# Performance work log

Hardware: AMD Instinct MI355X
Metric: run time of the kernel (lower is better)

The kernel has to match this reference:

```python
import jax, jax.numpy as jnp
import numpy as np

N, E = 50000, 200000          # nodes, edges
S, V = 256, 128               # 256x0e scalars, 128x1o vectors -> node dim 640
EDGE_DIM, HID = 64, 256
NUM_ATOM, NUM_BOND = 16, 5
FAN_TP = S * S + V * V        # fully-connected TP fan-in for rescale


def setup_inputs() -> dict:
    key = jax.random.key(0)
    ks = jax.random.split(key, 12)
    h_final = jax.random.normal(ks[0], (N, S + 3 * V), dtype=jnp.float32)
    e_final = jax.random.normal(ks[1], (E, EDGE_DIM), dtype=jnp.float32)
    target_node_mask = jnp.ones((N,), dtype=bool)
    target_edge_mask = jnp.ones((E,), dtype=bool)
    edge_index = jax.random.randint(ks[2], (2, E), 0, N)

    def lin(k, o, i):
        return (jax.random.normal(k, (o, i), jnp.float32) / np.sqrt(i)).astype(jnp.float32)

    return {
        "h_final": h_final,
        "e_final": e_final,
        "target_node_mask": target_node_mask,
        "target_edge_mask": target_edge_mask,
        "edge_index": edge_index,
        "Ws_w": lin(ks[3], S, S),          # LinearRS on scalar irreps (with bias)
        "Ws_b": jnp.zeros((S,), jnp.float32),
        "Wv": lin(ks[4], V, V),            # LinearRS on 1o irreps (no bias)
        "Wcoord": (jax.random.normal(ks[5], (V,), jnp.float32) / np.sqrt(V)),  # 128x1o -> 1x1o
        "W_tp00": jax.random.normal(ks[6], (S, S), jnp.float32),  # 0e x 0e -> 0e path weights
        "W_tp11": jax.random.normal(ks[7], (V, V), jnp.float32),  # 1o x 1o -> 0e path weights
        "atom_W1": lin(ks[8], HID, S), "atom_b1": jnp.zeros((HID,), jnp.float32),
        "atom_W2": lin(ks[9], NUM_ATOM, HID), "atom_b2": jnp.zeros((NUM_ATOM,), jnp.float32),
        "bond_W1": lin(ks[10], HID, 1 + EDGE_DIM), "bond_b1": jnp.zeros((HID,), jnp.float32),
        "bond_W2": lin(ks[11], NUM_BOND, HID), "bond_b2": jnp.zeros((NUM_BOND,), jnp.float32),
    }


def reference(h_final, e_final, target_node_mask, target_edge_mask, edge_index,
              Ws_w, Ws_b, Wv, Wcoord, W_tp00, W_tp11,
              atom_W1, atom_b1, atom_W2, atom_b2,
              bond_W1, bond_b1, bond_W2, bond_b2):
    # --- node heads (masks are all-True here; boolean gather kept for faithfulness) ---
    x = h_final[target_node_mask]                 # [Nt, 640]
    xs = x[:, :S]                                 # scalar (0e) part [Nt, 256]
    xv = x[:, S:].reshape(-1, V, 3)               # vector (1o) part [Nt, 128, 3]

    scalar_feats = xs @ Ws_w.T + Ws_b             # node_scalar_proj (LinearRS)
    atom_type_logits = jax.nn.silu(scalar_feats @ atom_W1.T + atom_b1) @ atom_W2.T + atom_b2

    vec = jnp.einsum('nci,dc->ndi', xv, Wv)       # node_vector_proj, per-component channel mix
    predicted_r0 = jnp.einsum('nci,c->ni', vec, Wcoord)  # coord_head -> [Nt, 3]

    # --- bond head: edge gather + fully-connected tensor product to 0e ---
    ei = edge_index[:, target_edge_mask]
    row, col = ei[0], ei[1]
    hr, hc = h_final[row], h_final[col]           # [Et, 640] each
    sr, sc = hr[:, :S], hc[:, :S]
    vr = hr[:, S:].reshape(-1, V, 3)
    vc = hc[:, S:].reshape(-1, V, 3)
    # paths: 0e(x)0e->0e and 1o(x)1o->0e (dot product, CG norm 1/sqrt(3)), rescaled by fan-in
    tp = (jnp.einsum('ei,ej,ij->e', sr, sc, W_tp00)
          + jnp.einsum('eci,edi,cd->e', vr, vc, W_tp11) / np.sqrt(3.0)) / np.sqrt(FAN_TP)
    bond_in = jnp.concatenate([tp[:, None], e_final[target_edge_mask]], axis=-1)  # [Et, 65]
    bond_logits = jax.nn.silu(bond_in @ bond_W1.T + bond_b1) @ bond_W2.T + bond_b2

    return atom_type_logits, predicted_r0, bond_logits
```

## Files before the change

### kernel.cpp

```cpp
#include <hip/hip_runtime.h>

typedef unsigned short u16;
typedef unsigned int u32;
typedef float f32x4 __attribute__((ext_vector_type(4)));
typedef float f32x2 __attribute__((ext_vector_type(2)));
typedef short s16x8 __attribute__((ext_vector_type(8)));
typedef __bf16 bf16x8 __attribute__((ext_vector_type(8)));

#define NNODE 50000
#define NEDGE 200000
#define INV_SQRT3 0.57735026918962576f
#define INV_SQRT_FAN 0.0034938562148434216f

__device__ inline float b2f(u16 x) {
    unsigned u = ((unsigned)x) << 16;
    return __builtin_bit_cast(float, u);
}
__device__ inline u16 f2b(float f) {
    unsigned u = __builtin_bit_cast(unsigned, f);
    unsigned r = u + 0x7FFFu + ((u >> 16) & 1u);
    return (u16)(r >> 16);
}
__device__ inline float silu(float v) { return v / (1.f + __expf(-v)); }

__device__ inline float ld1(const void* p, long i, int m) {
    return m ? ((const float*)p)[i] : b2f(((const u16*)p)[i]);
}
__device__ inline void stout(void* o, long i, float v, int m) {
    if (m) ((float*)o)[i] = v; else ((u16*)o)[i] = f2b(v);
}

#if defined(__has_builtin)
# if __has_builtin(__builtin_amdgcn_cvt_pk_f32_fp8) && __has_builtin(__builtin_amdgcn_cvt_pk_fp8_f32)
#  define HAVE_FP8 1
# endif
#endif
#ifndef HAVE_FP8
# define HAVE_FP8 0
#endif

__device__ inline int f2e4m3_soft(float f) {
    unsigned u = __builtin_bit_cast(unsigned, f);
    int s = (u >> 24) & 0x80;
    float a = __builtin_fabsf(f);
    if (a >= 464.f) return s | 0x7E;
    if (a < 0.015625f) {
        int q = (int)(a * 512.f + 0.5f);
        return s | q;
    }
    int e = (int)((u >> 23) & 0xFF) - 127;
    unsigned m = u & 0x7FFFFF;
    unsigned mq = (m + 0x80000) >> 20;
    if (mq == 8) { mq = 0; e += 1; }
    if (e > 8) return s | 0x7E;
    return s | ((e + 7) << 3) | (int)mq;
}
__device__ inline float e4m3f_soft(int b) {
    int em = b & 0x7F;
    float v;
    if (em >> 3) {
        unsigned bits = ((unsigned)((em >> 3) + 120) << 23) | ((unsigned)(em & 7) << 20);
        v = __builtin_bit_cast(float, bits);
    } else {
        v = (float)em * 0.001953125f;
    }
    return (b & 0x80) ? -v : v;
}
__device__ inline int enc2(float a, float b) {
#if HAVE_FP8
    return __builtin_amdgcn_cvt_pk_fp8_f32(a, b, 0, false) & 0xFFFF;
#else
    return f2e4m3_soft(a) | (f2e4m3_soft(b) << 8);
#endif
}
__device__ inline unsigned char enc1(float a) { return (unsigned char)(enc2(a, a) & 0xFF); }

__device__ inline float dot8(unsigned p, unsigned x, float acc) {
#if HAVE_FP8
    f32x2 p0 = __builtin_amdgcn_cvt_pk_f32_fp8((int)p, false);
    f32x2 p1 = __builtin_amdgcn_cvt_pk_f32_fp8((int)p, true);
    f32x2 x0 = __builtin_amdgcn_cvt_pk_f32_fp8((int)x, false);
    f32x2 x1 = __builtin_amdgcn_cvt_pk_f32_fp8((int)x, true);
    return acc + p0.x * x0.x + p0.y * x0.y + p1.x * x1.x + p1.y * x1.y;
#else
    float r = acc;
#pragma unroll
    for (int i = 0; i < 4; ++i)
        r += e4m3f_soft((p >> (8 * i)) & 0xFF) * e4m3f_soft((x >> (8 * i)) & 0xFF);
    return r;
#endif
}

template <typename V>
__device__ auto mfma_sel(V a, V b, f32x4 c, int)
    -> decltype(__builtin_amdgcn_mfma_f32_16x16x32_bf16(a, b, c, 0, 0, 0)) {
    return __builtin_amdgcn_mfma_f32_16x16x32_bf16(a, b, c, 0, 0, 0);
}
template <typename V>
__device__ f32x4 mfma_sel(V a, V b, f32x4 c, long) {
    bf16x8 aa = __builtin_bit_cast(bf16x8, a);
    bf16x8 bb = __builtin_bit_cast(bf16x8, b);
    return __builtin_amdgcn_mfma_f32_16x16x32_bf16(aa, bb, c, 0, 0, 0);
}
__device__ inline f32x4 mfma_bf16(s16x8 a, s16x8 b, f32x4 c) {
    return mfma_sel(a, b, c, 0);
}

typedef __attribute__((address_space(1))) u32 AS1u32;
typedef __attribute__((address_space(3))) u32 AS3u32;
__device__ __forceinline__ void async16(const void* g, void* l) {
    __builtin_amdgcn_global_load_lds((AS1u32*)g, (AS3u32*)l, 16, 0, 0);
}

__global__ __launch_bounds__(256) void detect_k(const void* __restrict__ h, int* __restrict__ flag) {
    int t = threadIdx.x;
    u16 w = ((const u16*)h)[2 * t];
    int tb = (w >> 8) & 0x7F;
    bool pl = (tb >= 0x38 && tb <= 0x41);
    unsigned long long b = __ballot(pl);
    __shared__ int cnt[4];
    if ((t & 63) == 0) cnt[t >> 6] = __popcll(b);
    __syncthreads();
    if (t == 0) {
        int s = cnt[0] + cnt[1] + cnt[2] + cnt[3];
        flag[0] = (s < 128) ? 1 : 0;
    }
}

__global__ __launch_bounds__(256) void prep_misc_k(
    const void* __restrict__ W00, const void* __restrict__ W11,
    const void* __restrict__ bW1, const void* __restrict__ Wv,
    const void* __restrict__ Wcoord, const void* __restrict__ aW2,
    const void* __restrict__ bW2, const void* __restrict__ bb1,
    u16* __restrict__ W00T, u16* __restrict__ W1p, u16* __restrict__ W2p,
    float* __restrict__ w1tp, float* __restrict__ w_eff,
    u16* __restrict__ W2ah, u16* __restrict__ W11T, float* __restrict__ b1f,
    const int* __restrict__ mflag)
{
    const int m = *mflag;
    int u = blockIdx.x * 256 + threadIdx.x;
    if (u < 65536) {
        int j = u >> 8, i = u & 255;
        W00T[u] = f2b(ld1(W00, (long)i * 256 + j, m));
    } else if (u < 81920) {
        int v = u - 65536;
        int j = v & 7, ln = (v >> 3) & 63, tk = v >> 9;
        int tn = tk >> 1, kt = tk & 1;
        int hrow = tn * 16 + (ln & 15);
        int k = kt * 32 + (ln >> 4) * 8 + j;
        W1p[v] = f2b(ld1(bW1, (long)hrow * 65 + 1 + k, m));
    } else if (u < 86016) {
        int v = u - 81920;
        int j = v & 7, ln = (v >> 3) & 63, kt = v >> 9;
        int o = ln & 15;
        int k = kt * 32 + (ln >> 4) * 8 + j;
        W2p[v] = (o < 5) ? f2b(ld1(bW2, (long)o * 256 + k, m)) : (u16)0;
    } else if (u < 86272) {
        int hd = u - 86016;
        w1tp[hd] = ld1(bW1, (long)hd * 65, m);
    } else if (u < 86400) {
        int c = u - 86272;
        float acc = 0.f;
        for (int d = 0; d < 128; ++d)
            acc += ld1(Wcoord, d, m) * ld1(Wv, (long)d * 128 + c, m);
        w_eff[c] = acc;
    } else if (u < 90496) {
        int v = u - 86400;
        W2ah[v] = f2b(ld1(aW2, v, m));
    } else if (u < 106880) {
        int v = u - 90496;
        int d = v >> 7, c = v & 127;
        W11T[v] = f2b(ld1(W11, (long)c * 128 + d, m));
    } else if (u < 107136) {
        int hd = u - 106880;
        b1f[hd] = ld1(bb1, hd, m);
    }
}

__global__ __launch_bounds__(256) void prep_w1s_k(
    const void* __restrict__ aW1, const void* __restrict__ Wsw,
    const void* __restrict__ Wsb, const void* __restrict__ ab1,
    u16* __restrict__ W1sh, float* __restrict__ b1p,
    const int* __restrict__ mflag)
{
    const int m = *mflag;
    int hd = blockIdx.x, s = threadIdx.x;
    float acc = 0.f;
    for (int j = 0; j < 256; ++j)
        acc += ld1(aW1, (long)hd * 256 + j, m) * ld1(Wsw, (long)j * 256 + s, m);
    W1sh[hd * 256 + s] = f2b(acc);
    if (s == 0) {
        float b = ld1(ab1, hd, m);
        for (int j = 0; j < 256; ++j)
            b += ld1(aW1, (long)hd * 256 + j, m) * ld1(Wsb, j, m);
        b1p[hd] = b;
    }
}

__global__ __launch_bounds__(256) void zero_k(float4* __restrict__ p) {
    int t = blockIdx.x * 256 + threadIdx.x;
    if (t < 200000) p[t] = float4{0.f, 0.f, 0.f, 0.f};
}

__device__ __forceinline__ void gemm_core_128(
    const u16* __restrict__ Aptr, int lda,
    const u16* __restrict__ Bt, int ldb, int bcol0,
    long bm0, int K, u16* __restrict__ S, f32x4 acc[4][4])
{
    u16* As = S;
    u16* Bs = S + 8192;
    int tid = threadIdx.x;
    int lane = tid & 63, wave = tid >> 6;
    int sr = lane >> 2, sc = (lane & 3) * 8;

    auto stage = [&](int buf, int k0) {
#pragma unroll
        for (int i = 0; i < 2; ++i) {
            int row = wave * 32 + i * 16 + sr;
            async16(Bt + (long)(bcol0 + row) * ldb + k0 + sc,
                    Bs + buf * 4096 + wave * 1024 + i * 512);
            long grow = bm0 + row; if (grow >= NNODE) grow = NNODE - 1;
            async16(Aptr + grow * (long)lda + k0 + sc,
                    As + buf * 4096 + wave * 1024 + i * 512);
        }
    };

    int NT = K >> 5;
    stage(0, 0);
    __syncthreads();
    int wm = (wave & 1) * 64, wn = (wave >> 1) * 64;
    int lm = lane & 15, quad = lane >> 4;
    for (int t = 0; t < NT; ++t) {
        int cur = t & 1;
        if (t + 1 < NT) stage(cur ^ 1, (t + 1) * 32);
        const u16* Ac = As + cur * 4096;
        const u16* Bc = Bs + cur * 4096;
        s16x8 af[4], bfr[4];
#pragma unroll
        for (int q = 0; q < 4; ++q) {
            af[q]  = *(const s16x8*)(Ac + (wm + q * 16 + lm) * 32 + quad * 8);
            bfr[q] = *(const s16x8*)(Bc + (wn + q * 16 + lm) * 32 + quad * 8);
        }
#pragma unroll
        for (int i = 0; i < 4; ++i)
#pragma unroll
            for (int j = 0; j < 4; ++j)
                acc[i][j] = mfma_bf16(af[i], bfr[j], acc[i][j]);
        __syncthreads();
    }
}

__global__ __launch_bounds__(256) void mlp1_k(
    const u16* __restrict__ Xs16, const u16* __restrict__ Bh,
    const float* __restrict__ b1p, const u16* __restrict__ W2ah,
    float* __restrict__ outP)
{
    __shared__ __align__(16) u16 S[17408];
    int bid = blockIdx.x;
    int x = bid & 7, s = bid >> 3;
    int rb = (s >> 1) * 8 + x, cb = s & 1;
    if (rb >= 391) return;
    long bm0 = (long)rb * 128;
    int bn0 = cb * 128;
    f32x4 acc[4][4] = {};
    gemm_core_128(Xs16, 256, Bh, 256, bn0, bm0, 256, S, acc);

    int tid = threadIdx.x, lane = tid & 63, wave = tid >> 6;
    int wm = (wave & 1) * 64, wn = (wave >> 1) * 64;
    int lm = lane & 15, quad = lane >> 4;
#pragma unroll
    for (int j = 0; j < 4; ++j) {
        int col = wn + j * 16 + lm;
        float bb = b1p[bn0 + col];
#pragma unroll
        for (int i = 0; i < 4; ++i)
#pragma unroll
            for (int rr = 0; rr < 4; ++rr)
                S[(wm + i * 16 + quad * 4 + rr) * 136 + col] = f2b(silu(acc[i][j][rr] + bb));
    }
    __syncthreads();
    const u16* wp = W2ah + lm * 256 + bn0;
#pragma unroll
    for (int rg = 0; rg < 2; ++rg) {
        int r0 = wave * 32 + rg * 16;
        f32x4 a2 = {0.f, 0.f, 0.f, 0.f};
#pragma unroll
        for (int k0 = 0; k0 < 128; k0 += 32) {
            s16x8 a = *(const s16x8*)(S + (r0 + lm) * 136 + k0 + quad * 8);
            s16x8 b = *(const s16x8*)(wp + k0 + quad * 8);
            a2 = mfma_bf16(a, b, a2);
        }
#pragma unroll
        for (int rr = 0; rr < 4; ++rr) {
            long grow = bm0 + r0 + quad * 4 + rr;
            if (grow < NNODE)
                atomicAdd(outP + grow * 16 + lm, a2[rr]);
        }
    }
}

__global__ __launch_bounds__(256) void fin_atom_k(
    const float* __restrict__ outP, const void* __restrict__ b2v,
    void* __restrict__ out, const int* __restrict__ mflag)
{
    const int m = *mflag;
    int t4 = blockIdx.x * 256 + threadIdx.x;
    if (t4 >= 200000) return;
    float4 v = *(const float4*)(outP + (long)t4 * 4);
    int b0i = (t4 * 4) & 15;
    float r0 = v.x + ld1(b2v, b0i + 0, m);
    float r1 = v.y + ld1(b2v, b0i + 1, m);
    float r2 = v.z + ld1(b2v, b0i + 2, m);
    float r3 = v.w + ld1(b2v, b0i + 3, m);
    if (m) {
        *(float4*)((float*)out + (long)t4 * 4) = float4{r0, r1, r2, r3};
    } else {
        u16 pk[4] = {f2b(r0), f2b(r1), f2b(r2), f2b(r3)};
        *(ushort4*)((u16*)out + (long)t4 * 4) = *(const ushort4*)pk;
    }
}

__global__ __launch_bounds__(256) void packx8_k(
    const void* __restrict__ h, u16* __restrict__ xvp,
    const float* __restrict__ w_eff, unsigned char* __restrict__ X8,
    u16* __restrict__ Xs16, void* __restrict__ out,
    const int* __restrict__ mflag)
{
    const int m = *mflag;
    int lane = threadIdx.x & 63, w = threadIdx.x >> 6;
    int node = blockIdx.x * 4 + w;
    if (node >= NNODE) return;
    float s4[4];
    if (m) {
        float4 v = *(const float4*)((const float*)h + (long)node * 640 + lane * 4);
        s4[0] = v.x; s4[1] = v.y; s4[2] = v.z; s4[3] = v.w;
    } else {
        ushort4 v = *(const ushort4*)((const u16*)h + (long)node * 640 + lane * 4);
        s4[0] = b2f(v.x); s4[1] = b2f(v.y); s4[2] = b2f(v.z); s4[3] = b2f(v.w);
    }
    unsigned sp = (unsigned)enc2(s4[0], s4[1]) | ((unsigned)enc2(s4[2], s4[3]) << 16);
    *(unsigned*)(X8 + (long)node * 640 + lane * 4) = sp;
    u16 sx[4] = {f2b(s4[0]), f2b(s4[1]), f2b(s4[2]), f2b(s4[3])};
    *(ushort4*)(Xs16 + (long)node * 256 + lane * 4) = *(const ushort4*)sx;
    float a[6];
    if (m) {
        const float* p = (const float*)h + (long)node * 640 + 256 + lane * 6;
        float2 v0 = *(const float2*)p;
        float2 v1 = *(const float2*)(p + 2);
        float2 v2 = *(const float2*)(p + 4);
        a[0] = v0.x; a[1] = v0.y; a[2] = v1.x; a[3] = v1.y; a[4] = v2.x; a[5] = v2.y;
    } else {
        const u16* p = (const u16*)h + (long)node * 640 + 256 + lane * 6;
        ushort2 v0 = *(const ushort2*)p;
        ushort2 v1 = *(const ushort2*)(p + 2);
        ushort2 v2 = *(const ushort2*)(p + 4);
        a[0] = b2f(v0.x); a[1] = b2f(v0.y); a[2] = b2f(v1.x);
        a[3] = b2f(v1.y); a[4] = b2f(v2.x); a[5] = b2f(v2.y);
    }
#pragma unroll
    for (int z = 0; z < 3; ++z) {
        unsigned pk = (unsigned)f2b(a[z]) | ((unsigned)f2b(a[z + 3]) << 16);
        *(unsigned*)(xvp + (long)z * 6400000 + (long)node * 128 + lane * 2) = pk;
        *(unsigned short*)(X8 + (long)node * 640 + 256 + z * 128 + lane * 2) =
            (unsigned short)enc2(a[z], a[z + 3]);
    }
    float2 we = *(const float2*)(w_eff + lane * 2);
    float s0 = a[0] * we.x + a[3] * we.y;
    float s1 = a[1] * we.x + a[4] * we.y;
    float s2 = a[2] * we.x + a[5] * we.y;
#pragma unroll
    for (int off = 32; off > 0; off >>= 1) {
        s0 += __shfl_down(s0, off);
        s1 += __shfl_down(s1, off);
        s2 += __shfl_down(s2, off);
    }
    if (lane == 0) {
        stout(out, 800000L + (long)node * 3 + 0, s0, m);
        stout(out, 800000L + (long)node * 3 + 1, s1, m);
        stout(out, 800000L + (long)node * 3 + 2, s2, m);
    }
}

__global__ __launch_bounds__(256) void gemm8n_k(
    const u16* __restrict__ Xs16, const u16* __restrict__ xvp,
    const u16* __restrict__ W00T, const u16* __restrict__ W11T,
    unsigned char* __restrict__ PQ8, float s00, float s11)
{
    __shared__ __align__(16) u16 S[16384];
    int bid = blockIdx.x;
    int x = bid & 7, s = bid >> 3;
    int rb = (s / 5) * 8 + x, cb = s % 5;
    if (rb >= 391) return;
    const bool qp = (cb >= 2);
    int z = cb - 2;
    long bm0 = (long)rb * 128;
    f32x4 acc[4][4] = {};
    if (qp)
        gemm_core_128(xvp + (long)z * 6400000, 128, W11T, 128, 0, bm0, 128, S, acc);
    else
        gemm_core_128(Xs16, 256, W00T, 256, cb * 128, bm0, 256, S, acc);

    float scale = qp ? s11 : s00;
    int colbase = qp ? (256 + z * 128) : cb * 128;
    unsigned char* C8 = (unsigned char*)S;
    int tid = threadIdx.x, lane = tid & 63, wave = tid >> 6;
    int wm = (wave & 1) * 64, wn = (wave >> 1) * 64;
    int lm = lane & 15, quad = lane >> 4;
#pragma unroll
    for (int j = 0; j < 4; ++j) {
        int col = wn + j * 16 + lm;
#pragma unroll
        for (int i = 0; i < 4; ++i)
#pragma unroll
            for (int rr = 0; rr < 4; ++rr) {
                int row = wm + i * 16 + quad * 4 + rr;
                C8[row * 128 + col] = enc1(scale * acc[i][j][rr]);
            }
    }
    __syncthreads();
#pragma unroll
    for (int v = 0; v < 4; ++v) {
        int idx = v * 256 + tid;
        int row = idx >> 3, seg = idx & 7;
        long grow = bm0 + row;
        if (grow < NNODE)
            *(uint4*)(PQ8 + grow * 640 + colbase + seg * 16) =
                *(const uint4*)(C8 + row * 128 + seg * 16);
    }
}

__global__ __launch_bounds__(256) void bond_fused_k(
    const void* __restrict__ A, const u16* __restrict__ W1p,
    const float* __restrict__ b1f, const u16* __restrict__ W2p,
    const void* __restrict__ b2v, const float* __restrict__ tp,
    const float* __restrict__ w1tp, void* __restrict__ out, long obase,
    const int* __restrict__ mflag)
{
    const int m = *mflag;
    __shared__ __align__(16) u16 hidS[4][16][264];
    int tid = threadIdx.x, lane = tid & 63, w = tid >> 6;
    int lm = lane & 15, quad = lane >> 4;
    int e0 = (blockIdx.x * 4 + w) * 16;
    s16x8 af0, af1;
    long base = (long)(e0 + lm) * 64 + quad * 8;
    if (m) {
        const float* ap = (const float*)A + base;
        float4 a0 = *(const float4*)ap,        a1 = *(const float4*)(ap + 4);
        float4 a2 = *(const float4*)(ap + 32), a3 = *(const float4*)(ap + 36);
        u16 t0[8] = {f2b(a0.x), f2b(a0.y), f2b(a0.z), f2b(a0.w),
                     f2b(a1.x), f2b(a1.y), f2b(a1.z), f2b(a1.w)};
        u16 t1[8] = {f2b(a2.x), f2b(a2.y), f2b(a2.z), f2b(a2.w),
                     f2b(a3.x), f2b(a3.y), f2b(a3.z), f2b(a3.w)};
        af0 = *(const s16x8*)t0; af1 = *(const s16x8*)t1;
    } else {
        af0 = *(const s16x8*)((const u16*)A + base);
        af1 = *(const s16x8*)((const u16*)A + base + 32);
    }
    float tpe = tp[e0 + lm];
    f32x4 acc1[16];
#pragma unroll
    for (int tn = 0; tn < 16; ++tn) {
        s16x8 b0 = *(const s16x8*)(W1p + ((tn * 2 + 0) * 64 + lane) * 8);
        s16x8 b1w = *(const s16x8*)(W1p + ((tn * 2 + 1) * 64 + lane) * 8);
        f32x4 a = {0.f, 0.f, 0.f, 0.f};
        a = mfma_bf16(b0, af0, a);
        a = mfma_bf16(b1w, af1, a);
        acc1[tn] = a;
    }
#pragma unroll
    for (int tn = 0; tn < 16; ++tn) {
        int hc0 = tn * 16 + quad * 4;
        float4 bb = *(const float4*)(b1f + hc0);
        float4 wt = *(const float4*)(w1tp + hc0);
        u16 pk[4];
        pk[0] = f2b(silu(acc1[tn][0] + bb.x + tpe * wt.x));
        pk[1] = f2b(silu(acc1[tn][1] + bb.y + tpe * wt.y));
        pk[2] = f2b(silu(acc1[tn][2] + bb.z + tpe * wt.z));
        pk[3] = f2b(silu(acc1[tn][3] + bb.w + tpe * wt.w));
        *(ushort4*)&hidS[w][lm][hc0] = *(const ushort4*)pk;
    }
    f32x4 acc2 = {0.f, 0.f, 0.f, 0.f};
#pragma unroll
    for (int kt = 0; kt < 8; ++kt) {
        s16x8 a = *(const s16x8*)&hidS[w][lm][kt * 32 + quad * 8];
        s16x8 b = *(const s16x8*)(W2p + (kt * 64 + lane) * 8);
        acc2 = mfma_bf16(a, b, acc2);
    }
    if (lm < 5) {
        float b2 = ld1(b2v, lm, m);
#pragma unroll
        for (int rr = 0; rr < 4; ++rr) {
            int e = e0 + quad * 4 + rr;
            stout(out, obase + (long)e * 5 + lm, acc2[rr] + b2, m);
        }
    }
}

__global__ __launch_bounds__(256) void tp_k(
    const int* __restrict__ ei, const unsigned char* __restrict__ PQ8,
    const unsigned char* __restrict__ X8, float* __restrict__ tp)
{
    int tid = threadIdx.x;
    int sub = tid & 15;
    int e = blockIdx.x * 16 + (tid >> 4);
    if (e >= NEDGE) return;
    int row = ei[e], col = ei[NEDGE + e];
    const unsigned char* pq = PQ8 + (long)row * 640;
    const unsigned char* xp = X8 + (long)col * 640;
    uint4 p0 = *(const uint4*)(pq + sub * 16);
    uint4 x0 = *(const uint4*)(xp + sub * 16);
    uint4 p1 = *(const uint4*)(pq + 256 + sub * 16);
    uint4 x1 = *(const uint4*)(xp + 256 + sub * 16);
    uint2 p2 = *(const uint2*)(pq + 512 + sub * 8);
    uint2 x2 = *(const uint2*)(xp + 512 + sub * 8);
    float acc = 0.f;
    acc = dot8(p0.x, x0.x, acc); acc = dot8(p0.y, x0.y, acc);
    acc = dot8(p0.z, x0.z, acc); acc = dot8(p0.w, x0.w, acc);
    acc = dot8(p1.x, x1.x, acc); acc = dot8(p1.y, x1.y, acc);
    acc = dot8(p1.z, x1.z, acc); acc = dot8(p1.w, x1.w, acc);
    acc = dot8(p2.x, x2.x, acc); acc = dot8(p2.y, x2.y, acc);
#pragma unroll
    for (int off = 8; off > 0; off >>= 1) acc += __shfl_down(acc, off);
    if (sub == 0) tp[e] = acc * 0.0625f;
}

extern "C" void kernel_launch(void* const* d_in, const int* in_sizes, int n_in,
                              void* d_out, int out_size, void* d_ws, size_t ws_size,
                              hipStream_t stream) {
    (void)in_sizes; (void)n_in; (void)out_size; (void)ws_size;
    const void* h      = d_in[0];
    const void* e_fin  = d_in[1];
    const int*  ei     = (const int*)d_in[4];
    const void* Ws_w   = d_in[5];
    const void* Ws_b   = d_in[6];
    const void* Wv     = d_in[7];
    const void* Wcoord = d_in[8];
    const void* W00    = d_in[9];
    const void* W11    = d_in[10];
    const void* aW1    = d_in[11];
    const void* ab1    = d_in[12];
    const void* aW2    = d_in[13];
    const void* ab2    = d_in[14];
    const void* bW1    = d_in[15];
    const void* bb1    = d_in[16];
    const void* bW2    = d_in[17];
    const void* bb2    = d_in[18];

    char* ws = (char*)d_ws;
    int*   mflag = (int*)(ws + 0);
    float* w1tp  = (float*)(ws + 512);
    float* w_eff = (float*)(ws + 2048);
    float* b1p   = (float*)(ws + 3072);
    u16*   W00T  = (u16*)(ws + 4096);
    u16*   W1p   = (u16*)(ws + 135168);
    u16*   W2p   = (u16*)(ws + 167936);
    u16*   W1sh  = (u16*)(ws + 176128);
    u16*   W2ah  = (u16*)(ws + 307200);
    u16*   W11T  = (u16*)(ws + 315392);
    float* tp    = (float*)(ws + 348160);
    float* b1f   = (float*)(ws + 1148160);
    char*  R     = ws + 1149184;
    unsigned char* PQ8  = (unsigned char*)R;
    unsigned char* X8   = (unsigned char*)(R + 33554432);
    u16*           xvp  = (u16*)(R + 67108864);
    u16*           Xs16 = (u16*)(R + 105906176);
    float*         outP = (float*)(R + 132120576);

    detect_k<<<1, 256, 0, stream>>>(h, mflag);
    prep_misc_k<<<419, 256, 0, stream>>>(W00, W11, bW1, Wv, Wcoord, aW2, bW2, bb1,
                                         W00T, W1p, W2p, w1tp, w_eff,
                                         W2ah, W11T, b1f, mflag);
    prep_w1s_k<<<256, 256, 0, stream>>>(aW1, Ws_w, Ws_b, ab1, W1sh, b1p, mflag);
    zero_k<<<782, 256, 0, stream>>>((float4*)outP);

    packx8_k<<<12500, 256, 0, stream>>>(h, xvp, w_eff, X8, Xs16, d_out, mflag);

    mlp1_k<<<784, 256, 0, stream>>>(Xs16, W1sh, b1p, W2ah, outP);
    fin_atom_k<<<782, 256, 0, stream>>>(outP, ab2, d_out, mflag);

    gemm8n_k<<<1960, 256, 0, stream>>>(Xs16, xvp, W00T, W11T, PQ8,
                                       16.f * INV_SQRT_FAN,
                                       16.f * INV_SQRT_FAN * INV_SQRT3);
    tp_k<<<12500, 256, 0, stream>>>(ei, PQ8, X8, tp);

    bond_fused_k<<<3125, 256, 0, stream>>>(e_fin, W1p, b1f, W2p, bb2,
                                           tp, w1tp, d_out, 950000L, mflag);
}
```

Measured before the change: 483.5 us.

## Merge atom MLP and TP projection GEMMs into one launch, read bf16 input directly

Merges the atom-head MLP GEMM and the TP projection GEMM into a single grid with seven column blocks per row tile. When the input is already bf16, the scalar operand is read straight from h with a stride of 640, so packx8 no longer writes the Xs16 copy in that mode. The prep_w1s bias reduction is also rewritten as a parallel shuffle reduction, and the inner loop is split into four accumulators. The aim is to cut launch overhead, fill the GPU with one larger grid, and avoid a redundant write. The cost is a more branchy kernel whose heterogeneous blocks share the same LDS size.

```diff
diff --git a/kernel.cpp b/kernel.cpp
--- a/kernel.cpp
+++ b/kernel.cpp
@@ -185,16 +185,26 @@
 {
     const int m = *mflag;
     int hd = blockIdx.x, s = threadIdx.x;
-    float acc = 0.f;
-    for (int j = 0; j < 256; ++j)
-        acc += ld1(aW1, (long)hd * 256 + j, m) * ld1(Wsw, (long)j * 256 + s, m);
-    W1sh[hd * 256 + s] = f2b(acc);
-    if (s == 0) {
-        float b = ld1(ab1, hd, m);
-        for (int j = 0; j < 256; ++j)
-            b += ld1(aW1, (long)hd * 256 + j, m) * ld1(Wsb, j, m);
-        b1p[hd] = b;
-    }
+    float a0 = 0.f, a1 = 0.f, a2 = 0.f, a3 = 0.f;
+    for (int j = 0; j < 256; j += 4) {
+        float w0 = ld1(aW1, (long)hd * 256 + j + 0, m);
+        float w1 = ld1(aW1, (long)hd * 256 + j + 1, m);
+        float w2 = ld1(aW1, (long)hd * 256 + j + 2, m);
+        float w3 = ld1(aW1, (long)hd * 256 + j + 3, m);
+        a0 += w0 * ld1(Wsw, (long)(j + 0) * 256 + s, m);
+        a1 += w1 * ld1(Wsw, (long)(j + 1) * 256 + s, m);
+        a2 += w2 * ld1(Wsw, (long)(j + 2) * 256 + s, m);
+        a3 += w3 * ld1(Wsw, (long)(j + 3) * 256 + s, m);
+    }
+    W1sh[hd * 256 + s] = f2b((a0 + a1) + (a2 + a3));
+    float pb = ld1(aW1, (long)hd * 256 + s, m) * ld1(Wsb, s, m);
+#pragma unroll
+    for (int off = 32; off > 0; off >>= 1) pb += __shfl_down(pb, off);
+    __shared__ float red[4];
+    if ((s & 63) == 0) red[s >> 6] = pb;
+    __syncthreads();
+    if (s == 0)
+        b1p[hd] = ld1(ab1, hd, m) + red[0] + red[1] + red[2] + red[3];
 }
 
 __global__ __launch_bounds__(256) void zero_k(float4* __restrict__ p) {
@@ -250,52 +260,96 @@
     }
 }
 
-__global__ __launch_bounds__(256) void mlp1_k(
-    const u16* __restrict__ Xs16, const u16* __restrict__ Bh,
-    const float* __restrict__ b1p, const u16* __restrict__ W2ah,
-    float* __restrict__ outP)
+__global__ __launch_bounds__(256) void gemmC_k(
+    const void* __restrict__ h, const u16* __restrict__ Xs16,
+    const u16* __restrict__ xvp,
+    const u16* __restrict__ W1sh, const float* __restrict__ b1p,
+    const u16* __restrict__ W2ah, float* __restrict__ outP,
+    const u16* __restrict__ W00T, const u16* __restrict__ W11T,
+    unsigned char* __restrict__ PQ8, float s00, float s11,
+    const int* __restrict__ mflag)
 {
     __shared__ __align__(16) u16 S[17408];
     int bid = blockIdx.x;
     int x = bid & 7, s = bid >> 3;
-    int rb = (s >> 1) * 8 + x, cb = s & 1;
+    int rb = (s / 7) * 8 + x, cb = s % 7;
     if (rb >= 391) return;
+    const int m = *mflag;
+    const u16* Ascal = m ? Xs16 : (const u16*)h;
+    const int ldas = m ? 256 : 640;
     long bm0 = (long)rb * 128;
-    int bn0 = cb * 128;
+
     f32x4 acc[4][4] = {};
-    gemm_core_128(Xs16, 256, Bh, 256, bn0, bm0, 256, S, acc);
-
     int tid = threadIdx.x, lane = tid & 63, wave = tid >> 6;
     int wm = (wave & 1) * 64, wn = (wave >> 1) * 64;
     int lm = lane & 15, quad = lane >> 4;
+
+    if (cb < 2) {
+        int bn0 = cb * 128;
+        gemm_core_128(Ascal, ldas, W1sh, 256, bn0, bm0, 256, S, acc);
+#pragma unroll
+        for (int j = 0; j < 4; ++j) {
+            int col = wn + j * 16 + lm;
+            float bb = b1p[bn0 + col];
+#pragma unroll
+            for (int i = 0; i < 4; ++i)
+#pragma unroll
+                for (int rr = 0; rr < 4; ++rr)
+                    S[(wm + i * 16 + quad * 4 + rr) * 136 + col] =
+                        f2b(silu(acc[i][j][rr] + bb));
+        }
+        __syncthreads();
+        const u16* wp = W2ah + lm * 256 + bn0;
+#pragma unroll
+        for (int rg = 0; rg < 2; ++rg) {
+            int r0 = wave * 32 + rg * 16;
+            f32x4 a2 = {0.f, 0.f, 0.f, 0.f};
+#pragma unroll
+            for (int k0 = 0; k0 < 128; k0 += 32) {
+                s16x8 a = *(const s16x8*)(S + (r0 + lm) * 136 + k0 + quad * 8);
+                s16x8 b = *(const s16x8*)(wp + k0 + quad * 8);
+                a2 = mfma_bf16(a, b, a2);
+            }
+#pragma unroll
+            for (int rr = 0; rr < 4; ++rr) {
+                long grow = bm0 + r0 + quad * 4 + rr;
+                if (grow < NNODE)
+                    atomicAdd(outP + grow * 16 + lm, a2[rr]);
+            }
+        }
+        return;
+    }
+
+    const bool qp = (cb >= 4);
+    int z = cb - 4;
+    if (qp)
+        gemm_core_128(xvp + (long)z * 6400000, 128, W11T, 128, 0, bm0, 128, S, acc);
+    else
+        gemm_core_128(Ascal, ldas, W00T, 256, (cb - 2) * 128, bm0, 256, S, acc);
+
+    float scale = qp ? s11 : s00;
+    int colbase = qp ? (256 + z * 128) : (cb - 2) * 128;
+    unsigned char* C8 = (unsigned char*)S;
 #pragma unroll
     for (int j = 0; j < 4; ++j) {
         int col = wn + j * 16 + lm;
-        float bb = b1p[bn0 + col];
 #pragma unroll
         for (int i = 0; i < 4; ++i)
 #pragma unroll
-            for (int rr = 0; rr < 4; ++rr)
-                S[(wm + i * 16 + quad * 4 + rr) * 136 + col] = f2b(silu(acc[i][j][rr] + bb));
+            for (int rr = 0; rr < 4; ++rr) {
+                int row = wm + i * 16 + quad * 4 + rr;
+                C8[row * 128 + col] = enc1(scale * acc[i][j][rr]);
+            }
     }
     __syncthreads();
-    const u16* wp = W2ah + lm * 256 + bn0;
-#pragma unroll
-    for (int rg = 0; rg < 2; ++rg) {
-        int r0 = wave * 32 + rg * 16;
-        f32x4 a2 = {0.f, 0.f, 0.f, 0.f};
-#pragma unroll
-        for (int k0 = 0; k0 < 128; k0 += 32) {
-            s16x8 a = *(const s16x8*)(S + (r0 + lm) * 136 + k0 + quad * 8);
-            s16x8 b = *(const s16x8*)(wp + k0 + quad * 8);
-            a2 = mfma_bf16(a, b, a2);
-        }
-#pragma unroll
-        for (int rr = 0; rr < 4; ++rr) {
-            long grow = bm0 + r0 + quad * 4 + rr;
-            if (grow < NNODE)
-                atomicAdd(outP + grow * 16 + lm, a2[rr]);
-        }
+#pragma unroll
+    for (int v = 0; v < 4; ++v) {
+        int idx = v * 256 + tid;
+        int row = idx >> 3, seg = idx & 7;
+        long grow = bm0 + row;
+        if (grow < NNODE)
+            *(uint4*)(PQ8 + grow * 640 + colbase + seg * 16) =
+                *(const uint4*)(C8 + row * 128 + seg * 16);
     }
 }
 
@@ -334,14 +388,14 @@
     if (m) {
         float4 v = *(const float4*)((const float*)h + (long)node * 640 + lane * 4);
         s4[0] = v.x; s4[1] = v.y; s4[2] = v.z; s4[3] = v.w;
+        u16 sx[4] = {f2b(s4[0]), f2b(s4[1]), f2b(s4[2]), f2b(s4[3])};
+        *(ushort4*)(Xs16 + (long)node * 256 + lane * 4) = *(const ushort4*)sx;
     } else {
         ushort4 v = *(const ushort4*)((const u16*)h + (long)node * 640 + lane * 4);
         s4[0] = b2f(v.x); s4[1] = b2f(v.y); s4[2] = b2f(v.z); s4[3] = b2f(v.w);
     }
     unsigned sp = (unsigned)enc2(s4[0], s4[1]) | ((unsigned)enc2(s4[2], s4[3]) << 16);
     *(unsigned*)(X8 + (long)node * 640 + lane * 4) = sp;
-    u16 sx[4] = {f2b(s4[0]), f2b(s4[1]), f2b(s4[2]), f2b(s4[3])};
-    *(ushort4*)(Xs16 + (long)node * 256 + lane * 4) = *(const ushort4*)sx;
     float a[6];
     if (m) {
         const float* p = (const float*)h + (long)node * 640 + 256 + lane * 6;
@@ -378,54 +432,6 @@
         stout(out, 800000L + (long)node * 3 + 0, s0, m);
         stout(out, 800000L + (long)node * 3 + 1, s1, m);
         stout(out, 800000L + (long)node * 3 + 2, s2, m);
-    }
-}
-
-__global__ __launch_bounds__(256) void gemm8n_k(
-    const u16* __restrict__ Xs16, const u16* __restrict__ xvp,
-    const u16* __restrict__ W00T, const u16* __restrict__ W11T,
-    unsigned char* __restrict__ PQ8, float s00, float s11)
-{
-    __shared__ __align__(16) u16 S[16384];
-    int bid = blockIdx.x;
-    int x = bid & 7, s = bid >> 3;
-    int rb = (s / 5) * 8 + x, cb = s % 5;
-    if (rb >= 391) return;
-    const bool qp = (cb >= 2);
-    int z = cb - 2;
-    long bm0 = (long)rb * 128;
-    f32x4 acc[4][4] = {};
-    if (qp)
-        gemm_core_128(xvp + (long)z * 6400000, 128, W11T, 128, 0, bm0, 128, S, acc);
-    else
-        gemm_core_128(Xs16, 256, W00T, 256, cb * 128, bm0, 256, S, acc);
-
-    float scale = qp ? s11 : s00;
-    int colbase = qp ? (256 + z * 128) : cb * 128;
-    unsigned char* C8 = (unsigned char*)S;
-    int tid = threadIdx.x, lane = tid & 63, wave = tid >> 6;
-    int wm = (wave & 1) * 64, wn = (wave >> 1) * 64;
-    int lm = lane & 15, quad = lane >> 4;
-#pragma unroll
-    for (int j = 0; j < 4; ++j) {
-        int col = wn + j * 16 + lm;
-#pragma unroll
-        for (int i = 0; i < 4; ++i)
-#pragma unroll
-            for (int rr = 0; rr < 4; ++rr) {
-                int row = wm + i * 16 + quad * 4 + rr;
-                C8[row * 128 + col] = enc1(scale * acc[i][j][rr]);
-            }
-    }
-    __syncthreads();
-#pragma unroll
-    for (int v = 0; v < 4; ++v) {
-        int idx = v * 256 + tid;
-        int row = idx >> 3, seg = idx & 7;
-        long grow = bm0 + row;
-        if (grow < NNODE)
-            *(uint4*)(PQ8 + grow * 640 + colbase + seg * 16) =
-                *(const uint4*)(C8 + row * 128 + seg * 16);
     }
 }
 
@@ -575,12 +581,12 @@
 
     packx8_k<<<12500, 256, 0, stream>>>(h, xvp, w_eff, X8, Xs16, d_out, mflag);
 
-    mlp1_k<<<784, 256, 0, stream>>>(Xs16, W1sh, b1p, W2ah, outP);
+    gemmC_k<<<2744, 256, 0, stream>>>(h, Xs16, xvp, W1sh, b1p, W2ah, outP,
+                                      W00T, W11T, PQ8,
+                                      16.f * INV_SQRT_FAN,
+                                      16.f * INV_SQRT_FAN * INV_SQRT3, mflag);
     fin_atom_k<<<782, 256, 0, stream>>>(outP, ab2, d_out, mflag);
 
-    gemm8n_k<<<1960, 256, 0, stream>>>(Xs16, xvp, W00T, W11T, PQ8,
-                                       16.f * INV_SQRT_FAN,
-                                       16.f * INV_SQRT_FAN * INV_SQRT3);
     tp_k<<<12500, 256, 0, stream>>>(ei, PQ8, X8, tp);
 
     bond_fused_k<<<3125, 256, 0, stream>>>(e_fin, W1p, b1f, W2p, bb2,
```

After: 448.1 us. 1.08x faster.
